# Optimization experiments

Measured on AMD Instinct MI355X. Metric: run time of the kernel, lower is better.

## Reference

```python
import jax, jax.numpy as jnp
import numpy as np

N, E = 50000, 600000
IN_C, HID, OUT_C = 256, 128, 2
R, B, L = 7, 8, 3
ALPHA = 0.1


def _rgcn(x, src, dst, etype, comp, basis, root, bias):
    # comp: [R,B], basis: [B,d,d] -> per-relation weights W: [R,d,d]
    n, d = x.shape
    W = jnp.einsum('rb,bdf->rdf', comp, basis)
    # combined (dst, relation) segment id for per-relation mean aggregation
    seg = dst * R + etype
    msg = x[src]  # [E,d] gather
    s = jax.ops.segment_sum(msg, seg, num_segments=n * R)  # [N*R,d]
    cnt = jax.ops.segment_sum(jnp.ones((E,), x.dtype), seg, num_segments=n * R)
    agg = (s / jnp.maximum(cnt, 1.0)[:, None]).reshape(n, R, d)  # per-relation mean
    return x @ root + bias + jnp.einsum('nrd,rdf->nf', agg, W)


def setup_inputs() -> dict:
    key = jax.random.key(0)
    ks = jax.random.split(key, 10)
    sc = 0.05
    x = jax.random.normal(ks[0], (N, IN_C), dtype=jnp.float32)
    edge_index = jax.random.randint(ks[1], (2, E), 0, N)
    edge_type = jax.random.randint(ks[2], (E,), 0, R)
    # GPR temp init: alpha*(1-alpha)^k, last entry (1-alpha)^K
    temp = jnp.asarray(ALPHA * (1.0 - ALPHA) ** np.arange(L + 1), dtype=jnp.float32)
    temp = temp.at[-1].set((1.0 - ALPHA) ** L)
    lin1_w = jax.random.normal(ks[3], (IN_C, HID), jnp.float32) * sc
    lin1_b = jnp.zeros((HID,), jnp.float32)
    lin2_w = jax.random.normal(ks[4], (HID, OUT_C), jnp.float32) * sc
    lin2_b = jnp.zeros((OUT_C,), jnp.float32)
    comps = jax.random.normal(ks[5], (L, R, B), jnp.float32) * sc
    bases = jax.random.normal(ks[6], (L, B, HID, HID), jnp.float32) * sc
    roots = jax.random.normal(ks[7], (L, HID, HID), jnp.float32) * sc
    conv_biases = jnp.zeros((L, HID), jnp.float32)
    return dict(x=x, edge_index=edge_index, edge_type=edge_type, temp=temp,
                lin1_w=lin1_w, lin1_b=lin1_b, lin2_w=lin2_w, lin2_b=lin2_b,
                comps=comps, bases=bases, roots=roots, conv_biases=conv_biases)


def reference(x, edge_index, edge_type, temp, lin1_w, lin1_b, lin2_w, lin2_b,
              comps, bases, roots, conv_biases):
    src, dst = edge_index[0], edge_index[1]
    h = x @ lin1_w + lin1_b
    hidden = h * temp[0]
    cur = hidden
    for i in range(L):
        cur = _rgcn(cur, src, dst, edge_type, comps[i], bases[i], roots[i], conv_biases[i])
        if i < L - 1:
            cur = jax.nn.relu(cur)  # dropout p=0.4 is identity in eval mode
        hidden = hidden + temp[i + 1] * cur
    return hidden @ lin2_w + lin2_b
```

## Files before the change

kernel.cpp:

```cpp
#include <hip/hip_runtime.h>
#include <cstdint>


constexpr int N_NODES  = 50000;
constexpr int E_EDGES  = 600000;
constexpr int R_REL    = 7;
constexpr int HID      = 128;
constexpr int IN_C     = 256;
constexpr int L_LAYERS = 3;
constexpr int AGG_COLS = 896;
constexpr int K_CAT    = 1024;
constexpr int NR       = N_NODES * R_REL;
constexpr int SCANR_BLOCKS = (NR + 255) / 256;

#define DEVI __device__ __forceinline__

using short8  = __attribute__((ext_vector_type(8))) short;
using floatx4 = __attribute__((ext_vector_type(4))) float;

DEVI unsigned short f2bf(float f) {
  unsigned u = __float_as_uint(f);
  unsigned r = (u + 0x7FFFu + ((u >> 16) & 1u)) >> 16;
  return (unsigned short)r;
}
DEVI float bf2f(unsigned short h) { return __uint_as_float(((unsigned)h) << 16); }

__global__ __launch_bounds__(256) void cast_w1_kernel(
    const float* __restrict__ w1, unsigned short* __restrict__ w1T)
{
  int t = blockIdx.x * 256 + threadIdx.x;
  if (t >= HID * IN_C) return;
  int m = t >> 8, k = t & 255;
  w1T[m * IN_C + k] = f2bf(w1[k * HID + m]);
}

__global__ __launch_bounds__(256) void build_wcat2(
    const float* __restrict__ comps,
    const float* __restrict__ bases,
    const float* __restrict__ roots,
    unsigned short* __restrict__ wcat2T)
{
  int t = blockIdx.x * 256 + threadIdx.x;
  if (t >= L_LAYERS * 128 * K_CAT) return;
  int l   = t >> 17;
  int rem = t & 131071;
  int f   = rem >> 10;
  int k   = rem & 1023;
  float v;
  if (k < 128) {
    v = roots[((size_t)l * 128 + k) * 128 + f];
  } else {
    int r = (k - 128) >> 7, d = (k - 128) & 127;
    const float* cp = comps + ((size_t)l * R_REL + r) * 8;
    const float* bp = bases + (((size_t)l * 8) * 128 + d) * 128 + f;
    float s = 0.f;
#pragma unroll
    for (int b = 0; b < 8; ++b) s += cp[b] * bp[(size_t)b * 128 * 128];
    v = s;
  }
  wcat2T[t] = f2bf(v);
}

__global__ __launch_bounds__(256) void hist_kernel(
    const int* __restrict__ ei, const int* __restrict__ et,
    int* __restrict__ cntRel, int* __restrict__ erank)
{
  int e = blockIdx.x * 256 + threadIdx.x;
  if (e >= E_EDGES) return;
  int seg = ei[E_EDGES + e] * R_REL + et[e];
  erank[e] = atomicAdd(&cntRel[seg], 1);
}

__global__ __launch_bounds__(256) void scanA_kernel(
    const int* __restrict__ cnt, int* __restrict__ tmpOff,
    int* __restrict__ blockSums)
{
  __shared__ int s[256];
  int i = blockIdx.x * 256 + threadIdx.x;
  int v = (i < NR) ? cnt[i] : 0;
  s[threadIdx.x] = v;
  __syncthreads();
#pragma unroll
  for (int d = 1; d < 256; d <<= 1) {
    int t = (threadIdx.x >= d) ? s[threadIdx.x - d] : 0;
    __syncthreads();
    s[threadIdx.x] += t;
    __syncthreads();
  }
  if (i < NR) tmpOff[i] = s[threadIdx.x] - v;
  if (threadIdx.x == 255) blockSums[blockIdx.x] = s[255];
}

__global__ __launch_bounds__(256) void scanB_kernel(int* __restrict__ bs)
{
  __shared__ int s[256];
  __shared__ int carry;
  if (threadIdx.x == 0) carry = 0;
  __syncthreads();
  for (int base = 0; base < SCANR_BLOCKS; base += 256) {
    int cOld = carry;
    int i = base + threadIdx.x;
    int v = (i < SCANR_BLOCKS) ? bs[i] : 0;
    s[threadIdx.x] = v;
    __syncthreads();
#pragma unroll
    for (int d = 1; d < 256; d <<= 1) {
      int t = (threadIdx.x >= d) ? s[threadIdx.x - d] : 0;
      __syncthreads();
      s[threadIdx.x] += t;
      __syncthreads();
    }
    if (i < SCANR_BLOCKS) bs[i] = s[threadIdx.x] - v + cOld;
    __syncthreads();
    if (threadIdx.x == 0) carry = cOld + s[255];
    __syncthreads();
  }
}

__global__ __launch_bounds__(256) void scanC_kernel(
    const int* __restrict__ tmpOff, const int* __restrict__ blockSums,
    int* __restrict__ drs)
{
  int i = blockIdx.x * 256 + threadIdx.x;
  if (i < NR) drs[i] = tmpOff[i] + blockSums[blockIdx.x];
  if (i == 0) drs[NR] = E_EDGES;
}

__global__ __launch_bounds__(256) void place_kernel(
    const int* __restrict__ ei, const int* __restrict__ et,
    const int* __restrict__ drs, const int* __restrict__ erank,
    unsigned short* __restrict__ esrc)
{
  int e = blockIdx.x * 256 + threadIdx.x;
  if (e >= E_EDGES) return;
  int seg = ei[E_EDGES + e] * R_REL + et[e];
  int pos = drs[seg] + erank[e];
  esrc[pos] = (unsigned short)ei[e];
}

constexpr int AGG_NPF = 16;
__global__ __launch_bounds__(256) void agg_reg_kernel(
    const unsigned short* __restrict__ curA,
    const unsigned short* __restrict__ esrc,
    const int* __restrict__ drs,
    unsigned short* __restrict__ aggB)
{
  const int tid  = threadIdx.x;
  const int lane = tid & 63;
  const int dst  = blockIdx.x * 4 + (tid >> 6);
  if (dst >= N_NODES) return;
  const int segBase = dst * R_REL;

  int bnd = drs[segBase + (lane & 7)];
  const int a0    = __shfl(bnd, 0);
  const int total = __shfl(bnd, 7) - a0;

  int pk = 0;
  if (lane < total) pk = (int)esrc[a0 + lane];

  const unsigned* colp = (const unsigned*)curA + lane;
  unsigned* outp = (unsigned*)(aggB + (size_t)dst * AGG_COLS) + lane;

  int r = 0;
  int segStart = 0;
  int segEnd = __shfl(bnd, 1) - a0;
  float sx = 0.f, sy = 0.f;
  int pos = 0;

#define AGG_FLUSH()                                                        \
  while (r < R_REL && segEnd == pos) {                                     \
    int c = segEnd - segStart;                                             \
    float sc = (c > 0) ? 1.0f / (float)c : 0.f;                            \
    unsigned pck = (unsigned)f2bf(sx * sc) | ((unsigned)f2bf(sy * sc) << 16); \
    outp[r * 64] = pck;                                                    \
    sx = 0.f; sy = 0.f;                                                    \
    segStart = segEnd;                                                     \
    ++r;                                                                   \
    segEnd = (r < R_REL) ? (__shfl(bnd, r + 1) - a0) : 0x7FFFFFFF;         \
  }

  AGG_FLUSH();

  for (int base = 0; base < total; base += AGG_NPF) {
    const int cnt = min(total - base, AGG_NPF);
    unsigned v[AGG_NPF];
#pragma unroll
    for (int e = 0; e < AGG_NPF; ++e) {
      if (e < cnt) {
        int idx = base + e;
        int src = (idx < 64) ? __shfl(pk, idx) : (int)esrc[a0 + idx];
        v[e] = colp[src * 64];
      }
    }
#pragma unroll
    for (int e = 0; e < AGG_NPF; ++e) {
      if (e >= cnt) break;
      unsigned u = v[e];
      sx += __uint_as_float(u << 16);
      sy += __uint_as_float(u & 0xFFFF0000u);
      ++pos;
      AGG_FLUSH();
    }
  }
#undef AGG_FLUSH
}

__global__ __launch_bounds__(256) void gemm_lin1(
    const float* __restrict__ x,
    const unsigned short* __restrict__ BT,
    const float* __restrict__ bias,
    const float* __restrict__ temp,
    unsigned short* __restrict__ b0out)
{
  __shared__ unsigned short Atile[64][136];
  __shared__ unsigned short Btile[128][136];
  const int tid  = threadIdx.x;
  const int row0 = blockIdx.x * 64;
  const int lane = tid & 63;
  const int wid  = tid >> 6;
  const int wrow = (wid & 1) * 32;
  const int wcol = (wid >> 1) * 64;
  const int l15  = lane & 15;
  const int quad = lane >> 4;

  floatx4 acc[2][4] = {};

  for (int k0 = 0; k0 < IN_C; k0 += 128) {
#pragma unroll
    for (int it = 0; it < 4; ++it) {
      int chunk = it * 256 + tid;
      int r = chunk >> 4, cc = (chunk & 15) << 3;
      int grow = row0 + r;
      uint4 va = make_uint4(0u, 0u, 0u, 0u);
      if (grow < N_NODES) {
        const float* xp = x + (size_t)grow * IN_C + k0 + cc;
        float4 f0 = *(const float4*)xp;
        float4 f1 = *(const float4*)(xp + 4);
        va.x = (unsigned)f2bf(f0.x) | ((unsigned)f2bf(f0.y) << 16);
        va.y = (unsigned)f2bf(f0.z) | ((unsigned)f2bf(f0.w) << 16);
        va.z = (unsigned)f2bf(f1.x) | ((unsigned)f2bf(f1.y) << 16);
        va.w = (unsigned)f2bf(f1.z) | ((unsigned)f2bf(f1.w) << 16);
      }
      *(uint4*)(&Atile[r][cc]) = va;
    }
#pragma unroll
    for (int it = 0; it < 8; ++it) {
      int chunk = it * 256 + tid;
      int n = chunk >> 4, cc = (chunk & 15) << 3;
      *(uint4*)(&Btile[n][cc]) =
          *(const uint4*)(BT + (size_t)n * IN_C + k0 + cc);
    }
    __syncthreads();
#pragma unroll
    for (int ks = 0; ks < 4; ++ks) {
      int kc = ks * 32 + quad * 8;
      short8 af[2], bfr[4];
#pragma unroll
      for (int i = 0; i < 2; ++i)
        af[i] = *(const short8*)(&Atile[wrow + i * 16 + l15][kc]);
#pragma unroll
      for (int j = 0; j < 4; ++j)
        bfr[j] = *(const short8*)(&Btile[wcol + j * 16 + l15][kc]);
#pragma unroll
      for (int i = 0; i < 2; ++i)
#pragma unroll
        for (int j = 0; j < 4; ++j)
          acc[i][j] = __builtin_amdgcn_mfma_f32_16x16x32_bf16(
              af[i], bfr[j], acc[i][j], 0, 0, 0);
    }
    __syncthreads();
  }

  float t0 = temp[0];
#pragma unroll
  for (int i = 0; i < 2; ++i) {
    int lrow0 = wrow + i * 16 + quad * 4;
#pragma unroll
    for (int j = 0; j < 4; ++j) {
      int gcol = wcol + j * 16 + l15;
      float bb = bias[gcol];
#pragma unroll
      for (int r = 0; r < 4; ++r)
        Atile[lrow0 + r][gcol] = f2bf(t0 * (acc[i][j][r] + bb));
    }
  }
  __syncthreads();
#pragma unroll
  for (int it = 0; it < 4; ++it) {
    int chunk = it * 256 + tid;
    int r = chunk >> 4, cc = (chunk & 15) << 3;
    int grow = row0 + r;
    if (grow < N_NODES)
      *(uint4*)(b0out + (size_t)grow * HID + cc) = *(const uint4*)(&Atile[r][cc]);
  }
}

__global__ __launch_bounds__(256) void gemm_layer(
    const unsigned short* __restrict__ curA,
    const unsigned short* __restrict__ aggB,
    const unsigned short* __restrict__ BT,
    const float* __restrict__ bias,
    unsigned short* __restrict__ bout,
    int layer)
{
  __shared__ unsigned short Atile[64][136];
  __shared__ unsigned short Btile[128][136];
  const int tid  = threadIdx.x;
  const int row0 = blockIdx.x * 64;
  const int lane = tid & 63;
  const int wid  = tid >> 6;
  const int wrow = (wid & 1) * 32;
  const int wcol = (wid >> 1) * 64;
  const int l15  = lane & 15;
  const int quad = lane >> 4;

  floatx4 acc[2][4] = {};

  for (int p = 0; p < 8; ++p) {
#pragma unroll
    for (int it = 0; it < 8; ++it) {
      int chunk = it * 256 + tid;
      int n = chunk >> 4, cc = (chunk & 15) << 3;
      *(uint4*)(&Btile[n][cc]) =
          *(const uint4*)(BT + (size_t)n * K_CAT + p * 128 + cc);
    }
#pragma unroll
    for (int it = 0; it < 4; ++it) {
      int chunk = it * 256 + tid;
      int r = chunk >> 4, cc = (chunk & 15) << 3;
      int grow = row0 + r;
      uint4 va = make_uint4(0u, 0u, 0u, 0u);
      if (grow < N_NODES) {
        if (p == 0)
          va = *(const uint4*)(curA + (size_t)grow * HID + cc);
        else
          va = *(const uint4*)(aggB + (size_t)grow * AGG_COLS +
                               (p - 1) * 128 + cc);
      }
      *(uint4*)(&Atile[r][cc]) = va;
    }
    __syncthreads();
#pragma unroll
    for (int ks = 0; ks < 4; ++ks) {
      int kc = ks * 32 + quad * 8;
      short8 af[2], bfr[4];
#pragma unroll
      for (int i = 0; i < 2; ++i)
        af[i] = *(const short8*)(&Atile[wrow + i * 16 + l15][kc]);
#pragma unroll
      for (int j = 0; j < 4; ++j)
        bfr[j] = *(const short8*)(&Btile[wcol + j * 16 + l15][kc]);
#pragma unroll
      for (int i = 0; i < 2; ++i)
#pragma unroll
        for (int j = 0; j < 4; ++j)
          acc[i][j] = __builtin_amdgcn_mfma_f32_16x16x32_bf16(
              af[i], bfr[j], acc[i][j], 0, 0, 0);
    }
    __syncthreads();
  }

  const bool isLast = (layer == L_LAYERS - 1);
#pragma unroll
  for (int i = 0; i < 2; ++i) {
    int lrow0 = wrow + i * 16 + quad * 4;
#pragma unroll
    for (int j = 0; j < 4; ++j) {
      int gcol = wcol + j * 16 + l15;
      float bb = bias[gcol];
#pragma unroll
      for (int r = 0; r < 4; ++r) {
        float c = acc[i][j][r] + bb;
        if (!isLast) c = fmaxf(c, 0.f);
        Atile[lrow0 + r][gcol] = f2bf(c);
      }
    }
  }
  __syncthreads();
#pragma unroll
  for (int it = 0; it < 4; ++it) {
    int chunk = it * 256 + tid;
    int r = chunk >> 4, cc = (chunk & 15) << 3;
    int grow = row0 + r;
    if (grow < N_NODES)
      *(uint4*)(bout + (size_t)grow * HID + cc) = *(const uint4*)(&Atile[r][cc]);
  }
}

__global__ __launch_bounds__(256) void final_kernel(
    const unsigned short* __restrict__ b0, const unsigned short* __restrict__ b1,
    const unsigned short* __restrict__ b2v, const unsigned short* __restrict__ b3,
    const float* __restrict__ temp,
    const float* __restrict__ w2, const float* __restrict__ b2bias,
    float* __restrict__ out)
{
  int node = blockIdx.x * 4 + (threadIdx.x >> 6);
  int lane = threadIdx.x & 63;
  if (node >= N_NODES) return;
  float t1 = temp[1], t2 = temp[2], t3 = temp[3];
  size_t base = (size_t)node * 64 + lane;
  unsigned u0 = ((const unsigned*)b0)[base];
  unsigned u1 = ((const unsigned*)b1)[base];
  unsigned u2 = ((const unsigned*)b2v)[base];
  unsigned u3 = ((const unsigned*)b3)[base];
  float hx = bf2f((unsigned short)(u0 & 0xFFFF)) +
             t1 * bf2f((unsigned short)(u1 & 0xFFFF)) +
             t2 * bf2f((unsigned short)(u2 & 0xFFFF)) +
             t3 * bf2f((unsigned short)(u3 & 0xFFFF));
  float hy = bf2f((unsigned short)(u0 >> 16)) +
             t1 * bf2f((unsigned short)(u1 >> 16)) +
             t2 * bf2f((unsigned short)(u2 >> 16)) +
             t3 * bf2f((unsigned short)(u3 >> 16));
  int d0 = lane * 2, d1 = lane * 2 + 1;
  float a0 = hx * w2[d0 * 2 + 0] + hy * w2[d1 * 2 + 0];
  float a1 = hx * w2[d0 * 2 + 1] + hy * w2[d1 * 2 + 1];
#pragma unroll
  for (int off = 32; off > 0; off >>= 1) {
    a0 += __shfl_down(a0, off);
    a1 += __shfl_down(a1, off);
  }
  if (lane == 0) {
    out[node * 2 + 0] = a0 + b2bias[0];
    out[node * 2 + 1] = a1 + b2bias[1];
  }
}

extern "C" void kernel_launch(void* const* d_in, const int* in_sizes, int n_in,
                              void* d_out, int out_size, void* d_ws, size_t ws_size,
                              hipStream_t stream) {
  const float* x     = (const float*)d_in[0];
  const int*   ei    = (const int*)d_in[1];
  const int*   et    = (const int*)d_in[2];
  const float* temp  = (const float*)d_in[3];
  const float* w1    = (const float*)d_in[4];
  const float* b1    = (const float*)d_in[5];
  const float* w2    = (const float*)d_in[6];
  const float* b2    = (const float*)d_in[7];
  const float* comps = (const float*)d_in[8];
  const float* bases = (const float*)d_in[9];
  const float* roots = (const float*)d_in[10];
  const float* cbias = (const float*)d_in[11];

  char* ws = (char*)d_ws;
  size_t off = 0;
  auto take = [&](size_t bytes) {
    char* p = ws + off;
    off = (off + bytes + 255) & ~(size_t)255;
    return p;
  };
  unsigned short* wcat2T = (unsigned short*)take((size_t)L_LAYERS * 128 * K_CAT * 2);
  unsigned short* w1T    = (unsigned short*)take((size_t)HID * IN_C * 2);
  int*   cntRel  = (int*)take((size_t)NR * 4);
  int*   tmpOffR = (int*)take((size_t)NR * 4);
  int*   blockSumsR = (int*)take((size_t)SCANR_BLOCKS * 4);
  int*   drs     = (int*)take((size_t)(NR + 1) * 4);
  int*   erank   = (int*)take((size_t)E_EDGES * 4);
  unsigned short* esrc = (unsigned short*)take((size_t)E_EDGES * 2);
  unsigned short* bl[L_LAYERS + 1];
  for (int i = 0; i <= L_LAYERS; ++i)
    bl[i] = (unsigned short*)take((size_t)N_NODES * HID * 2);
  unsigned short* aggB = (unsigned short*)take((size_t)N_NODES * AGG_COLS * 2);

  hipMemsetAsync(cntRel, 0, (size_t)NR * 4, stream);

  hipLaunchKernelGGL(build_wcat2, dim3((L_LAYERS * 128 * K_CAT + 255) / 256),
                     dim3(256), 0, stream, comps, bases, roots, wcat2T);
  hipLaunchKernelGGL(cast_w1_kernel, dim3((HID * IN_C + 255) / 256), dim3(256),
                     0, stream, w1, w1T);
  hipLaunchKernelGGL(hist_kernel, dim3((E_EDGES + 255) / 256), dim3(256), 0,
                     stream, ei, et, cntRel, erank);
  hipLaunchKernelGGL(scanA_kernel, dim3(SCANR_BLOCKS), dim3(256), 0, stream,
                     cntRel, tmpOffR, blockSumsR);
  hipLaunchKernelGGL(scanB_kernel, dim3(1), dim3(256), 0, stream, blockSumsR);
  hipLaunchKernelGGL(scanC_kernel, dim3(SCANR_BLOCKS), dim3(256), 0, stream,
                     tmpOffR, blockSumsR, drs);
  hipLaunchKernelGGL(place_kernel, dim3((E_EDGES + 255) / 256), dim3(256), 0,
                     stream, ei, et, drs, erank, esrc);

  const int rowBlocks64 = (N_NODES + 63) / 64;
  hipLaunchKernelGGL(gemm_lin1, dim3(rowBlocks64), dim3(256), 0, stream,
                     x, w1T, b1, temp, bl[0]);

  for (int l = 0; l < L_LAYERS; ++l) {
    hipLaunchKernelGGL(agg_reg_kernel, dim3((N_NODES + 3) / 4), dim3(256),
                       0, stream, bl[l], esrc, drs, aggB);
    hipLaunchKernelGGL(gemm_layer, dim3(rowBlocks64), dim3(256), 0, stream,
                       bl[l], aggB, wcat2T + (size_t)l * 128 * K_CAT,
                       cbias + (size_t)l * HID, bl[l + 1], l);
  }

  hipLaunchKernelGGL(final_kernel, dim3((N_NODES + 3) / 4), dim3(256), 0, stream,
                     bl[0], bl[1], bl[2], bl[3], temp, w2, b2, (float*)d_out);
}
```

Baseline: 496.5 us.

## Fuse per-relation aggregation into layer GEMM via shared-memory tile

Merges the gather/mean aggregation kernel and the layer GEMM into one kernel. Each 512-thread block aggregates 16 destination nodes into a shared-memory [16 x 1024] bf16 tile, then runs MFMA against the concatenated weights. This removes the write and re-read of the large intermediate aggregation buffer and one launch per layer. In exchange, each block reloads the full 128x1024 weight matrix for only 16 rows, which raises weight traffic and leaves little MFMA work per block.

```diff
diff --git a/kernel.cpp b/kernel.cpp
--- a/kernel.cpp
+++ b/kernel.cpp
@@ -8,10 +8,10 @@
 constexpr int HID      = 128;
 constexpr int IN_C     = 256;
 constexpr int L_LAYERS = 3;
-constexpr int AGG_COLS = 896;
 constexpr int K_CAT    = 1024;
 constexpr int NR       = N_NODES * R_REL;
 constexpr int SCANR_BLOCKS = (NR + 255) / 256;
+constexpr int BLK_D    = 16;
 
 #define DEVI __device__ __forceinline__
 
@@ -136,73 +136,6 @@
   int seg = ei[E_EDGES + e] * R_REL + et[e];
   int pos = drs[seg] + erank[e];
   esrc[pos] = (unsigned short)ei[e];
-}
-
-constexpr int AGG_NPF = 16;
-__global__ __launch_bounds__(256) void agg_reg_kernel(
-    const unsigned short* __restrict__ curA,
-    const unsigned short* __restrict__ esrc,
-    const int* __restrict__ drs,
-    unsigned short* __restrict__ aggB)
-{
-  const int tid  = threadIdx.x;
-  const int lane = tid & 63;
-  const int dst  = blockIdx.x * 4 + (tid >> 6);
-  if (dst >= N_NODES) return;
-  const int segBase = dst * R_REL;
-
-  int bnd = drs[segBase + (lane & 7)];
-  const int a0    = __shfl(bnd, 0);
-  const int total = __shfl(bnd, 7) - a0;
-
-  int pk = 0;
-  if (lane < total) pk = (int)esrc[a0 + lane];
-
-  const unsigned* colp = (const unsigned*)curA + lane;
-  unsigned* outp = (unsigned*)(aggB + (size_t)dst * AGG_COLS) + lane;
-
-  int r = 0;
-  int segStart = 0;
-  int segEnd = __shfl(bnd, 1) - a0;
-  float sx = 0.f, sy = 0.f;
-  int pos = 0;
-
-#define AGG_FLUSH()                                                        \
-  while (r < R_REL && segEnd == pos) {                                     \
-    int c = segEnd - segStart;                                             \
-    float sc = (c > 0) ? 1.0f / (float)c : 0.f;                            \
-    unsigned pck = (unsigned)f2bf(sx * sc) | ((unsigned)f2bf(sy * sc) << 16); \
-    outp[r * 64] = pck;                                                    \
-    sx = 0.f; sy = 0.f;                                                    \
-    segStart = segEnd;                                                     \
-    ++r;                                                                   \
-    segEnd = (r < R_REL) ? (__shfl(bnd, r + 1) - a0) : 0x7FFFFFFF;         \
-  }
-
-  AGG_FLUSH();
-
-  for (int base = 0; base < total; base += AGG_NPF) {
-    const int cnt = min(total - base, AGG_NPF);
-    unsigned v[AGG_NPF];
-#pragma unroll
-    for (int e = 0; e < AGG_NPF; ++e) {
-      if (e < cnt) {
-        int idx = base + e;
-        int src = (idx < 64) ? __shfl(pk, idx) : (int)esrc[a0 + idx];
-        v[e] = colp[src * 64];
-      }
-    }
-#pragma unroll
-    for (int e = 0; e < AGG_NPF; ++e) {
-      if (e >= cnt) break;
-      unsigned u = v[e];
-      sx += __uint_as_float(u << 16);
-      sy += __uint_as_float(u & 0xFFFF0000u);
-      ++pos;
-      AGG_FLUSH();
-    }
-  }
-#undef AGG_FLUSH
 }
 
 __global__ __launch_bounds__(256) void gemm_lin1(
@@ -295,95 +228,124 @@
   }
 }
 
-__global__ __launch_bounds__(256) void gemm_layer(
+constexpr int AGG_NPF = 16;
+__global__ __launch_bounds__(512, 4) void fused_layer(
     const unsigned short* __restrict__ curA,
-    const unsigned short* __restrict__ aggB,
+    const unsigned short* __restrict__ esrc,
+    const int* __restrict__ drs,
     const unsigned short* __restrict__ BT,
     const float* __restrict__ bias,
     unsigned short* __restrict__ bout,
     int layer)
 {
-  __shared__ unsigned short Atile[64][136];
+  __shared__ unsigned short Mtile[BLK_D][1032];
   __shared__ unsigned short Btile[128][136];
   const int tid  = threadIdx.x;
-  const int row0 = blockIdx.x * 64;
   const int lane = tid & 63;
   const int wid  = tid >> 6;
-  const int wrow = (wid & 1) * 32;
-  const int wcol = (wid >> 1) * 64;
+  const int row0 = blockIdx.x * BLK_D;
   const int l15  = lane & 15;
   const int quad = lane >> 4;
 
-  floatx4 acc[2][4] = {};
-
+  if (tid < 256) {
+    int r = tid >> 4, cc = (tid & 15) << 3;
+    *(uint4*)(&Mtile[r][cc]) =
+        *(const uint4*)(curA + (size_t)(row0 + r) * HID + cc);
+  }
+
+  const unsigned* colp = (const unsigned*)curA + lane;
+#pragma unroll
+  for (int s = 0; s < 2; ++s) {
+    const int ld  = wid * 2 + s;
+    const int dst = row0 + ld;
+    int bnd = drs[dst * R_REL + (lane & 7)];
+    const int a0    = __shfl(bnd, 0);
+    const int total = __shfl(bnd, 7) - a0;
+    int pk = 0;
+    if (lane < total) pk = (int)esrc[a0 + lane];
+
+    int r = 0;
+    int segStart = 0;
+    int segEnd = __shfl(bnd, 1) - a0;
+    float sx = 0.f, sy = 0.f;
+    int pos = 0;
+
+#define AGG_FLUSH()                                                          \
+    while (r < R_REL && segEnd == pos) {                                     \
+      int c = segEnd - segStart;                                             \
+      float sc = (c > 0) ? 1.0f / (float)c : 0.f;                            \
+      unsigned pck = (unsigned)f2bf(sx * sc) | ((unsigned)f2bf(sy * sc) << 16); \
+      *(unsigned*)(&Mtile[ld][HID + r * HID + lane * 2]) = pck;              \
+      sx = 0.f; sy = 0.f;                                                    \
+      segStart = segEnd;                                                     \
+      ++r;                                                                   \
+      segEnd = (r < R_REL) ? (__shfl(bnd, r + 1) - a0) : 0x7FFFFFFF;         \
+    }
+
+    AGG_FLUSH();
+
+    for (int base = 0; base < total; base += AGG_NPF) {
+      const int cnt = min(total - base, AGG_NPF);
+      unsigned v[AGG_NPF];
+#pragma unroll
+      for (int e = 0; e < AGG_NPF; ++e) {
+        if (e < cnt) {
+          int idx = base + e;
+          int src = (idx < 64) ? __shfl(pk, idx) : (int)esrc[a0 + idx];
+          v[e] = colp[src * 64];
+        }
+      }
+#pragma unroll
+      for (int e = 0; e < AGG_NPF; ++e) {
+        if (e >= cnt) break;
+        unsigned u = v[e];
+        sx += __uint_as_float(u << 16);
+        sy += __uint_as_float(u & 0xFFFF0000u);
+        ++pos;
+        AGG_FLUSH();
+      }
+    }
+#undef AGG_FLUSH
+  }
+  __syncthreads();
+
+  floatx4 acc = {};
   for (int p = 0; p < 8; ++p) {
 #pragma unroll
-    for (int it = 0; it < 8; ++it) {
-      int chunk = it * 256 + tid;
+    for (int it = 0; it < 4; ++it) {
+      int chunk = it * 512 + tid;
       int n = chunk >> 4, cc = (chunk & 15) << 3;
       *(uint4*)(&Btile[n][cc]) =
           *(const uint4*)(BT + (size_t)n * K_CAT + p * 128 + cc);
     }
-#pragma unroll
-    for (int it = 0; it < 4; ++it) {
-      int chunk = it * 256 + tid;
-      int r = chunk >> 4, cc = (chunk & 15) << 3;
-      int grow = row0 + r;
-      uint4 va = make_uint4(0u, 0u, 0u, 0u);
-      if (grow < N_NODES) {
-        if (p == 0)
-          va = *(const uint4*)(curA + (size_t)grow * HID + cc);
-        else
-          va = *(const uint4*)(aggB + (size_t)grow * AGG_COLS +
-                               (p - 1) * 128 + cc);
-      }
-      *(uint4*)(&Atile[r][cc]) = va;
-    }
     __syncthreads();
 #pragma unroll
     for (int ks = 0; ks < 4; ++ks) {
       int kc = ks * 32 + quad * 8;
-      short8 af[2], bfr[4];
-#pragma unroll
-      for (int i = 0; i < 2; ++i)
-        af[i] = *(const short8*)(&Atile[wrow + i * 16 + l15][kc]);
-#pragma unroll
-      for (int j = 0; j < 4; ++j)
-        bfr[j] = *(const short8*)(&Btile[wcol + j * 16 + l15][kc]);
-#pragma unroll
-      for (int i = 0; i < 2; ++i)
-#pragma unroll
-        for (int j = 0; j < 4; ++j)
-          acc[i][j] = __builtin_amdgcn_mfma_f32_16x16x32_bf16(
-              af[i], bfr[j], acc[i][j], 0, 0, 0);
+      short8 af  = *(const short8*)(&Mtile[l15][p * 128 + kc]);
+      short8 bfr = *(const short8*)(&Btile[wid * 16 + l15][kc]);
+      acc = __builtin_amdgcn_mfma_f32_16x16x32_bf16(af, bfr, acc, 0, 0, 0);
     }
     __syncthreads();
   }
 
   const bool isLast = (layer == L_LAYERS - 1);
-#pragma unroll
-  for (int i = 0; i < 2; ++i) {
-    int lrow0 = wrow + i * 16 + quad * 4;
-#pragma unroll
-    for (int j = 0; j < 4; ++j) {
-      int gcol = wcol + j * 16 + l15;
-      float bb = bias[gcol];
-#pragma unroll
-      for (int r = 0; r < 4; ++r) {
-        float c = acc[i][j][r] + bb;
-        if (!isLast) c = fmaxf(c, 0.f);
-        Atile[lrow0 + r][gcol] = f2bf(c);
-      }
+  {
+    int lrow0 = quad * 4;
+    int gcol  = wid * 16 + l15;
+    float bb = bias[gcol];
+#pragma unroll
+    for (int r2 = 0; r2 < 4; ++r2) {
+      float c = acc[r2] + bb;
+      if (!isLast) c = fmaxf(c, 0.f);
+      Mtile[lrow0 + r2][gcol] = f2bf(c);
     }
   }
   __syncthreads();
-#pragma unroll
-  for (int it = 0; it < 4; ++it) {
-    int chunk = it * 256 + tid;
-    int r = chunk >> 4, cc = (chunk & 15) << 3;
-    int grow = row0 + r;
-    if (grow < N_NODES)
-      *(uint4*)(bout + (size_t)grow * HID + cc) = *(const uint4*)(&Atile[r][cc]);
+  if (tid < 256) {
+    int r = tid >> 4, cc = (tid & 15) << 3;
+    *(uint4*)(bout + (size_t)(row0 + r) * HID + cc) =
+        *(const uint4*)(&Mtile[r][cc]);
   }
 }
 
@@ -459,7 +421,6 @@
   unsigned short* bl[L_LAYERS + 1];
   for (int i = 0; i <= L_LAYERS; ++i)
     bl[i] = (unsigned short*)take((size_t)N_NODES * HID * 2);
-  unsigned short* aggB = (unsigned short*)take((size_t)N_NODES * AGG_COLS * 2);
 
   hipMemsetAsync(cntRel, 0, (size_t)NR * 4, stream);
 
@@ -482,10 +443,8 @@
                      x, w1T, b1, temp, bl[0]);
 
   for (int l = 0; l < L_LAYERS; ++l) {
-    hipLaunchKernelGGL(agg_reg_kernel, dim3((N_NODES + 3) / 4), dim3(256),
-                       0, stream, bl[l], esrc, drs, aggB);
-    hipLaunchKernelGGL(gemm_layer, dim3(rowBlocks64), dim3(256), 0, stream,
-                       bl[l], aggB, wcat2T + (size_t)l * 128 * K_CAT,
+    hipLaunchKernelGGL(fused_layer, dim3(N_NODES / BLK_D), dim3(512), 0, stream,
+                       bl[l], esrc, drs, wcat2T + (size_t)l * 128 * K_CAT,
                        cbias + (size_t)l * HID, bl[l + 1], l);
   }
 
```

Measured after the change: 638.0 us. +28.5%, slower.

## Fuse final projection into GEMM epilogues and merge weight prep kernels

Applied to the files above, without the earlier changes.

Removes the separate final kernel that re-read all four hidden buffers. Each GEMM epilogue now projects its bf16 tile through lin2 and accumulates the temp-weighted result into the output: lin1 writes it, each layer adds to it. The two weight-preparation kernels are also merged into one launch. The trade-off is extra per-block epilogue work and a read-modify-write of the output in every layer. Because the projection now reads the bf16-rounded values of the intermediate buffers, rounding behaviour differs slightly.

```diff
diff --git a/kernel.cpp b/kernel.cpp
--- a/kernel.cpp
+++ b/kernel.cpp
@@ -12,6 +12,7 @@
 constexpr int K_CAT    = 1024;
 constexpr int NR       = N_NODES * R_REL;
 constexpr int SCANR_BLOCKS = (NR + 255) / 256;
+constexpr int WCAT_ELEMS = L_LAYERS * 128 * K_CAT;
 
 #define DEVI __device__ __forceinline__
 
@@ -25,40 +26,40 @@
 }
 DEVI float bf2f(unsigned short h) { return __uint_as_float(((unsigned)h) << 16); }
 
-__global__ __launch_bounds__(256) void cast_w1_kernel(
-    const float* __restrict__ w1, unsigned short* __restrict__ w1T)
-{
-  int t = blockIdx.x * 256 + threadIdx.x;
-  if (t >= HID * IN_C) return;
-  int m = t >> 8, k = t & 255;
-  w1T[m * IN_C + k] = f2bf(w1[k * HID + m]);
-}
-
-__global__ __launch_bounds__(256) void build_wcat2(
+__global__ __launch_bounds__(256) void prep_weights(
+    const float* __restrict__ w1,
     const float* __restrict__ comps,
     const float* __restrict__ bases,
     const float* __restrict__ roots,
+    unsigned short* __restrict__ w1T,
     unsigned short* __restrict__ wcat2T)
 {
   int t = blockIdx.x * 256 + threadIdx.x;
-  if (t >= L_LAYERS * 128 * K_CAT) return;
-  int l   = t >> 17;
-  int rem = t & 131071;
-  int f   = rem >> 10;
-  int k   = rem & 1023;
-  float v;
-  if (k < 128) {
-    v = roots[((size_t)l * 128 + k) * 128 + f];
+  if (t < WCAT_ELEMS) {
+    int l   = t >> 17;
+    int rem = t & 131071;
+    int f   = rem >> 10;
+    int k   = rem & 1023;
+    float v;
+    if (k < 128) {
+      v = roots[((size_t)l * 128 + k) * 128 + f];
+    } else {
+      int r = (k - 128) >> 7, d = (k - 128) & 127;
+      const float* cp = comps + ((size_t)l * R_REL + r) * 8;
+      const float* bp = bases + (((size_t)l * 8) * 128 + d) * 128 + f;
+      float s = 0.f;
+#pragma unroll
+      for (int b = 0; b < 8; ++b) s += cp[b] * bp[(size_t)b * 128 * 128];
+      v = s;
+    }
+    wcat2T[t] = f2bf(v);
   } else {
-    int r = (k - 128) >> 7, d = (k - 128) & 127;
-    const float* cp = comps + ((size_t)l * R_REL + r) * 8;
-    const float* bp = bases + (((size_t)l * 8) * 128 + d) * 128 + f;
-    float s = 0.f;
-#pragma unroll
-    for (int b = 0; b < 8; ++b) s += cp[b] * bp[(size_t)b * 128 * 128];
-    v = s;
-  }
-  wcat2T[t] = f2bf(v);
+    int u = t - WCAT_ELEMS;
+    if (u < HID * IN_C) {
+      int m = u >> 8, k = u & 255;
+      w1T[m * IN_C + k] = f2bf(w1[k * HID + m]);
+    }
+  }
 }
 
 __global__ __launch_bounds__(256) void hist_kernel(
@@ -210,7 +211,10 @@
     const unsigned short* __restrict__ BT,
     const float* __restrict__ bias,
     const float* __restrict__ temp,
-    unsigned short* __restrict__ b0out)
+    const float* __restrict__ w2,
+    const float* __restrict__ b2bias,
+    unsigned short* __restrict__ b0out,
+    float* __restrict__ out)
 {
   __shared__ unsigned short Atile[64][136];
   __shared__ unsigned short Btile[128][136];
@@ -293,6 +297,30 @@
     if (grow < N_NODES)
       *(uint4*)(b0out + (size_t)grow * HID + cc) = *(const uint4*)(&Atile[r][cc]);
   }
+  {
+    int r = tid >> 2, q = tid & 3;
+    int grow = row0 + r;
+    float s0 = 0.f, s1 = 0.f;
+    if (grow < N_NODES) {
+#pragma unroll
+      for (int c8 = 0; c8 < 4; ++c8) {
+        short8 v = *(const short8*)(&Atile[r][q * 32 + c8 * 8]);
+#pragma unroll
+        for (int d = 0; d < 8; ++d) {
+          float f = bf2f((unsigned short)v[d]);
+          int col = q * 32 + c8 * 8 + d;
+          s0 += f * w2[col * 2 + 0];
+          s1 += f * w2[col * 2 + 1];
+        }
+      }
+    }
+    s0 += __shfl_xor(s0, 1); s1 += __shfl_xor(s1, 1);
+    s0 += __shfl_xor(s0, 2); s1 += __shfl_xor(s1, 2);
+    if (q == 0 && grow < N_NODES) {
+      out[grow * 2 + 0] = s0 + b2bias[0];
+      out[grow * 2 + 1] = s1 + b2bias[1];
+    }
+  }
 }
 
 __global__ __launch_bounds__(256) void gemm_layer(
@@ -300,7 +328,10 @@
     const unsigned short* __restrict__ aggB,
     const unsigned short* __restrict__ BT,
     const float* __restrict__ bias,
+    const float* __restrict__ temp,
+    const float* __restrict__ w2,
     unsigned short* __restrict__ bout,
+    float* __restrict__ out,
     int layer)
 {
   __shared__ unsigned short Atile[64][136];
@@ -385,43 +416,30 @@
     if (grow < N_NODES)
       *(uint4*)(bout + (size_t)grow * HID + cc) = *(const uint4*)(&Atile[r][cc]);
   }
-}
-
-__global__ __launch_bounds__(256) void final_kernel(
-    const unsigned short* __restrict__ b0, const unsigned short* __restrict__ b1,
-    const unsigned short* __restrict__ b2v, const unsigned short* __restrict__ b3,
-    const float* __restrict__ temp,
-    const float* __restrict__ w2, const float* __restrict__ b2bias,
-    float* __restrict__ out)
-{
-  int node = blockIdx.x * 4 + (threadIdx.x >> 6);
-  int lane = threadIdx.x & 63;
-  if (node >= N_NODES) return;
-  float t1 = temp[1], t2 = temp[2], t3 = temp[3];
-  size_t base = (size_t)node * 64 + lane;
-  unsigned u0 = ((const unsigned*)b0)[base];
-  unsigned u1 = ((const unsigned*)b1)[base];
-  unsigned u2 = ((const unsigned*)b2v)[base];
-  unsigned u3 = ((const unsigned*)b3)[base];
-  float hx = bf2f((unsigned short)(u0 & 0xFFFF)) +
-             t1 * bf2f((unsigned short)(u1 & 0xFFFF)) +
-             t2 * bf2f((unsigned short)(u2 & 0xFFFF)) +
-             t3 * bf2f((unsigned short)(u3 & 0xFFFF));
-  float hy = bf2f((unsigned short)(u0 >> 16)) +
-             t1 * bf2f((unsigned short)(u1 >> 16)) +
-             t2 * bf2f((unsigned short)(u2 >> 16)) +
-             t3 * bf2f((unsigned short)(u3 >> 16));
-  int d0 = lane * 2, d1 = lane * 2 + 1;
-  float a0 = hx * w2[d0 * 2 + 0] + hy * w2[d1 * 2 + 0];
-  float a1 = hx * w2[d0 * 2 + 1] + hy * w2[d1 * 2 + 1];
-#pragma unroll
-  for (int off = 32; off > 0; off >>= 1) {
-    a0 += __shfl_down(a0, off);
-    a1 += __shfl_down(a1, off);
-  }
-  if (lane == 0) {
-    out[node * 2 + 0] = a0 + b2bias[0];
-    out[node * 2 + 1] = a1 + b2bias[1];
+  {
+    float tl = temp[layer + 1];
+    int r = tid >> 2, q = tid & 3;
+    int grow = row0 + r;
+    float s0 = 0.f, s1 = 0.f;
+    if (grow < N_NODES) {
+#pragma unroll
+      for (int c8 = 0; c8 < 4; ++c8) {
+        short8 v = *(const short8*)(&Atile[r][q * 32 + c8 * 8]);
+#pragma unroll
+        for (int d = 0; d < 8; ++d) {
+          float f = bf2f((unsigned short)v[d]);
+          int col = q * 32 + c8 * 8 + d;
+          s0 += f * w2[col * 2 + 0];
+          s1 += f * w2[col * 2 + 1];
+        }
+      }
+    }
+    s0 += __shfl_xor(s0, 1); s1 += __shfl_xor(s1, 1);
+    s0 += __shfl_xor(s0, 2); s1 += __shfl_xor(s1, 2);
+    if (q == 0 && grow < N_NODES) {
+      out[grow * 2 + 0] += tl * s0;
+      out[grow * 2 + 1] += tl * s1;
+    }
   }
 }
 
@@ -448,7 +466,7 @@
     off = (off + bytes + 255) & ~(size_t)255;
     return p;
   };
-  unsigned short* wcat2T = (unsigned short*)take((size_t)L_LAYERS * 128 * K_CAT * 2);
+  unsigned short* wcat2T = (unsigned short*)take((size_t)WCAT_ELEMS * 2);
   unsigned short* w1T    = (unsigned short*)take((size_t)HID * IN_C * 2);
   int*   cntRel  = (int*)take((size_t)NR * 4);
   int*   tmpOffR = (int*)take((size_t)NR * 4);
@@ -463,10 +481,9 @@
 
   hipMemsetAsync(cntRel, 0, (size_t)NR * 4, stream);
 
-  hipLaunchKernelGGL(build_wcat2, dim3((L_LAYERS * 128 * K_CAT + 255) / 256),
-                     dim3(256), 0, stream, comps, bases, roots, wcat2T);
-  hipLaunchKernelGGL(cast_w1_kernel, dim3((HID * IN_C + 255) / 256), dim3(256),
-                     0, stream, w1, w1T);
+  hipLaunchKernelGGL(prep_weights,
+                     dim3((WCAT_ELEMS + HID * IN_C + 255) / 256), dim3(256),
+                     0, stream, w1, comps, bases, roots, w1T, wcat2T);
   hipLaunchKernelGGL(hist_kernel, dim3((E_EDGES + 255) / 256), dim3(256), 0,
                      stream, ei, et, cntRel, erank);
   hipLaunchKernelGGL(scanA_kernel, dim3(SCANR_BLOCKS), dim3(256), 0, stream,
@@ -479,16 +496,14 @@
 
   const int rowBlocks64 = (N_NODES + 63) / 64;
   hipLaunchKernelGGL(gemm_lin1, dim3(rowBlocks64), dim3(256), 0, stream,
-                     x, w1T, b1, temp, bl[0]);
+                     x, w1T, b1, temp, w2, b2, bl[0], (float*)d_out);
 
   for (int l = 0; l < L_LAYERS; ++l) {
     hipLaunchKernelGGL(agg_reg_kernel, dim3((N_NODES + 3) / 4), dim3(256),
                        0, stream, bl[l], esrc, drs, aggB);
     hipLaunchKernelGGL(gemm_layer, dim3(rowBlocks64), dim3(256), 0, stream,
                        bl[l], aggB, wcat2T + (size_t)l * 128 * K_CAT,
-                       cbias + (size_t)l * HID, bl[l + 1], l);
-  }
-
-  hipLaunchKernelGGL(final_kernel, dim3((N_NODES + 3) / 4), dim3(256), 0, stream,
-                     bl[0], bl[1], bl[2], bl[3], temp, w2, b2, (float*)d_out);
-}
+                       cbias + (size_t)l * HID, temp, w2, bl[l + 1],
+                       (float*)d_out, l);
+  }
+}
```

Measured after the change: 517.5 us. 4.2% more time.

## Aggregate per (dst, relation) segment with one wave each; fuse weight prep kernels

Applied to the files above, without the earlier changes.

Replaces the per-destination aggregation kernel, where one wavefront walked all seven relation segments with shuffled prefetched sources and a flush macro, with a simpler kernel that assigns one wavefront to each (dst, relation) segment and loops over its edges directly. This gives seven times more wavefronts and removes the serial flush logic, but each wave now handles only about 1.7 edges, loads its source indices one at a time without batching, and launches many waves for empty segments. It also merges the w1 cast and the per-layer weight build into one launch to save a kernel launch.

```diff
diff --git a/kernel.cpp b/kernel.cpp
--- a/kernel.cpp
+++ b/kernel.cpp
@@ -12,6 +12,7 @@
 constexpr int K_CAT    = 1024;
 constexpr int NR       = N_NODES * R_REL;
 constexpr int SCANR_BLOCKS = (NR + 255) / 256;
+constexpr int WCAT_ELEMS = L_LAYERS * 128 * K_CAT;
 
 #define DEVI __device__ __forceinline__
 
@@ -25,40 +26,40 @@
 }
 DEVI float bf2f(unsigned short h) { return __uint_as_float(((unsigned)h) << 16); }
 
-__global__ __launch_bounds__(256) void cast_w1_kernel(
-    const float* __restrict__ w1, unsigned short* __restrict__ w1T)
-{
-  int t = blockIdx.x * 256 + threadIdx.x;
-  if (t >= HID * IN_C) return;
-  int m = t >> 8, k = t & 255;
-  w1T[m * IN_C + k] = f2bf(w1[k * HID + m]);
-}
-
-__global__ __launch_bounds__(256) void build_wcat2(
+__global__ __launch_bounds__(256) void prep_weights(
+    const float* __restrict__ w1,
     const float* __restrict__ comps,
     const float* __restrict__ bases,
     const float* __restrict__ roots,
+    unsigned short* __restrict__ w1T,
     unsigned short* __restrict__ wcat2T)
 {
   int t = blockIdx.x * 256 + threadIdx.x;
-  if (t >= L_LAYERS * 128 * K_CAT) return;
-  int l   = t >> 17;
-  int rem = t & 131071;
-  int f   = rem >> 10;
-  int k   = rem & 1023;
-  float v;
-  if (k < 128) {
-    v = roots[((size_t)l * 128 + k) * 128 + f];
+  if (t < WCAT_ELEMS) {
+    int l   = t >> 17;
+    int rem = t & 131071;
+    int f   = rem >> 10;
+    int k   = rem & 1023;
+    float v;
+    if (k < 128) {
+      v = roots[((size_t)l * 128 + k) * 128 + f];
+    } else {
+      int r = (k - 128) >> 7, d = (k - 128) & 127;
+      const float* cp = comps + ((size_t)l * R_REL + r) * 8;
+      const float* bp = bases + (((size_t)l * 8) * 128 + d) * 128 + f;
+      float s = 0.f;
+#pragma unroll
+      for (int b = 0; b < 8; ++b) s += cp[b] * bp[(size_t)b * 128 * 128];
+      v = s;
+    }
+    wcat2T[t] = f2bf(v);
   } else {
-    int r = (k - 128) >> 7, d = (k - 128) & 127;
-    const float* cp = comps + ((size_t)l * R_REL + r) * 8;
-    const float* bp = bases + (((size_t)l * 8) * 128 + d) * 128 + f;
-    float s = 0.f;
-#pragma unroll
-    for (int b = 0; b < 8; ++b) s += cp[b] * bp[(size_t)b * 128 * 128];
-    v = s;
-  }
-  wcat2T[t] = f2bf(v);
+    int u = t - WCAT_ELEMS;
+    if (u < HID * IN_C) {
+      int m = u >> 8, k = u & 255;
+      w1T[m * IN_C + k] = f2bf(w1[k * HID + m]);
+    }
+  }
 }
 
 __global__ __launch_bounds__(256) void hist_kernel(
@@ -138,71 +139,31 @@
   esrc[pos] = (unsigned short)ei[e];
 }
 
-constexpr int AGG_NPF = 16;
-__global__ __launch_bounds__(256) void agg_reg_kernel(
+__global__ __launch_bounds__(256) void agg_seg_kernel(
     const unsigned short* __restrict__ curA,
     const unsigned short* __restrict__ esrc,
     const int* __restrict__ drs,
     unsigned short* __restrict__ aggB)
 {
-  const int tid  = threadIdx.x;
-  const int lane = tid & 63;
-  const int dst  = blockIdx.x * 4 + (tid >> 6);
-  if (dst >= N_NODES) return;
-  const int segBase = dst * R_REL;
-
-  int bnd = drs[segBase + (lane & 7)];
-  const int a0    = __shfl(bnd, 0);
-  const int total = __shfl(bnd, 7) - a0;
-
-  int pk = 0;
-  if (lane < total) pk = (int)esrc[a0 + lane];
+  const int lane = threadIdx.x & 63;
+  const int seg  = blockIdx.x * 4 + (threadIdx.x >> 6);
+  if (seg >= NR) return;
+  const int a = drs[seg];
+  const int b = drs[seg + 1];
 
   const unsigned* colp = (const unsigned*)curA + lane;
-  unsigned* outp = (unsigned*)(aggB + (size_t)dst * AGG_COLS) + lane;
-
-  int r = 0;
-  int segStart = 0;
-  int segEnd = __shfl(bnd, 1) - a0;
   float sx = 0.f, sy = 0.f;
-  int pos = 0;
-
-#define AGG_FLUSH()                                                        \
-  while (r < R_REL && segEnd == pos) {                                     \
-    int c = segEnd - segStart;                                             \
-    float sc = (c > 0) ? 1.0f / (float)c : 0.f;                            \
-    unsigned pck = (unsigned)f2bf(sx * sc) | ((unsigned)f2bf(sy * sc) << 16); \
-    outp[r * 64] = pck;                                                    \
-    sx = 0.f; sy = 0.f;                                                    \
-    segStart = segEnd;                                                     \
-    ++r;                                                                   \
-    segEnd = (r < R_REL) ? (__shfl(bnd, r + 1) - a0) : 0x7FFFFFFF;         \
-  }
-
-  AGG_FLUSH();
-
-  for (int base = 0; base < total; base += AGG_NPF) {
-    const int cnt = min(total - base, AGG_NPF);
-    unsigned v[AGG_NPF];
-#pragma unroll
-    for (int e = 0; e < AGG_NPF; ++e) {
-      if (e < cnt) {
-        int idx = base + e;
-        int src = (idx < 64) ? __shfl(pk, idx) : (int)esrc[a0 + idx];
-        v[e] = colp[src * 64];
-      }
-    }
-#pragma unroll
-    for (int e = 0; e < AGG_NPF; ++e) {
-      if (e >= cnt) break;
-      unsigned u = v[e];
-      sx += __uint_as_float(u << 16);
-      sy += __uint_as_float(u & 0xFFFF0000u);
-      ++pos;
-      AGG_FLUSH();
-    }
-  }
-#undef AGG_FLUSH
+  for (int e = a; e < b; ++e) {
+    int src = (int)esrc[e];
+    unsigned u = colp[(size_t)src * 64];
+    sx += __uint_as_float(u << 16);
+    sy += __uint_as_float(u & 0xFFFF0000u);
+  }
+  int c = b - a;
+  float sc = (c > 0) ? 1.0f / (float)c : 0.f;
+  unsigned pck = (unsigned)f2bf(sx * sc) | ((unsigned)f2bf(sy * sc) << 16);
+  int dst = seg / R_REL, r = seg - dst * R_REL;
+  ((unsigned*)aggB)[(size_t)dst * (AGG_COLS / 2) + r * 64 + lane] = pck;
 }
 
 __global__ __launch_bounds__(256) void gemm_lin1(
@@ -448,7 +409,7 @@
     off = (off + bytes + 255) & ~(size_t)255;
     return p;
   };
-  unsigned short* wcat2T = (unsigned short*)take((size_t)L_LAYERS * 128 * K_CAT * 2);
+  unsigned short* wcat2T = (unsigned short*)take((size_t)WCAT_ELEMS * 2);
   unsigned short* w1T    = (unsigned short*)take((size_t)HID * IN_C * 2);
   int*   cntRel  = (int*)take((size_t)NR * 4);
   int*   tmpOffR = (int*)take((size_t)NR * 4);
@@ -463,10 +424,9 @@
 
   hipMemsetAsync(cntRel, 0, (size_t)NR * 4, stream);
 
-  hipLaunchKernelGGL(build_wcat2, dim3((L_LAYERS * 128 * K_CAT + 255) / 256),
-                     dim3(256), 0, stream, comps, bases, roots, wcat2T);
-  hipLaunchKernelGGL(cast_w1_kernel, dim3((HID * IN_C + 255) / 256), dim3(256),
-                     0, stream, w1, w1T);
+  hipLaunchKernelGGL(prep_weights,
+                     dim3((WCAT_ELEMS + HID * IN_C + 255) / 256), dim3(256),
+                     0, stream, w1, comps, bases, roots, w1T, wcat2T);
   hipLaunchKernelGGL(hist_kernel, dim3((E_EDGES + 255) / 256), dim3(256), 0,
                      stream, ei, et, cntRel, erank);
   hipLaunchKernelGGL(scanA_kernel, dim3(SCANR_BLOCKS), dim3(256), 0, stream,
@@ -482,7 +442,7 @@
                      x, w1T, b1, temp, bl[0]);
 
   for (int l = 0; l < L_LAYERS; ++l) {
-    hipLaunchKernelGGL(agg_reg_kernel, dim3((N_NODES + 3) / 4), dim3(256),
+    hipLaunchKernelGGL(agg_seg_kernel, dim3((NR + 3) / 4), dim3(256),
                        0, stream, bl[l], esrc, drs, aggB);
     hipLaunchKernelGGL(gemm_layer, dim3(rowBlocks64), dim3(256), 0, stream,
                        bl[l], aggB, wcat2T + (size_t)l * 128 * K_CAT,
```

Measured after the change: 602.3 us. 1.21x slower.
